# Kernel tuning notes

Measured on AMD Instinct MI355X. Metric: run time of the kernel, lower is better.

## Reference

```python
import jax, jax.numpy as jnp
import numpy as np

N = 100000       # nodes
E = 1600000      # edges (avg degree 16)
F_IN = 128
F_HID = 64
F_OUT = 40
K = 10
ALPHA = 0.1


def setup_inputs() -> dict:
    key = jax.random.key(0)
    k1, k2, k3, k4, k5, k6 = jax.random.split(key, 6)
    x = jax.random.normal(k1, (N, F_IN), dtype=jnp.float32)
    edge_index = jax.random.randint(k2, (2, E), 0, N, dtype=jnp.int32)
    # Linear params (Kaiming-uniform-ish scale)
    W1 = jax.random.normal(k3, (F_IN, F_HID), dtype=jnp.float32) / np.sqrt(F_IN)
    b1 = jax.random.normal(k4, (F_HID,), dtype=jnp.float32) * 0.01
    W2 = jax.random.normal(k5, (F_HID, F_OUT), dtype=jnp.float32) / np.sqrt(F_HID)
    b2 = jax.random.normal(k6, (F_OUT,), dtype=jnp.float32) * 0.01
    return {"x": x, "edge_index": edge_index, "W1": W1, "b1": b1, "W2": W2, "b2": b2}


def _gcn_norm(edge_index, dtype):
    # add self loops, symmetric normalization D^{-1/2} (A+I) D^{-1/2}
    loops = jnp.arange(N, dtype=edge_index.dtype)
    src = jnp.concatenate([edge_index[0], loops])
    dst = jnp.concatenate([edge_index[1], loops])
    deg = jax.ops.segment_sum(jnp.ones_like(src, dtype=dtype), dst, num_segments=N)
    dinv = jnp.where(deg > 0, jax.lax.rsqrt(deg), 0.0).astype(dtype)
    norm = dinv[src] * dinv[dst]  # [E + N]
    return src, dst, norm


def _appnp(x, src, dst, norm):
    h = x  # teleport target
    def step(xc, _):
        agg = jax.ops.segment_sum(xc[src] * norm[:, None], dst, num_segments=N)
        return (1.0 - ALPHA) * agg + ALPHA * h, None
    out, _ = jax.lax.scan(step, x, None, length=K)
    return out


def reference(x, edge_index, W1, b1, W2, b2):
    src, dst, norm = _gcn_norm(edge_index, x.dtype)
    # layer 1: Linear -> relu -> (dropout p=0) -> APPNP
    h = jax.nn.relu(x @ W1 + b1)
    h = _appnp(h, src, dst, norm)
    # layer 2: Linear -> relu -> APPNP
    h = jax.nn.relu(h @ W2 + b2)
    h = _appnp(h, src, dst, norm)
    return jax.nn.log_softmax(h, axis=1)
```

## Files before the change

kernel.cpp:

```cpp
#include <hip/hip_runtime.h>
#include <hip/hip_fp16.h>
#include <hip/hip_fp8.h>

namespace {
constexpr int NN = 100000;
constexpr int NE = 1600000;
constexpr int FIN = 128, FHID = 64, FOUT = 40;
constexpr float ALPHA = 0.1f;
constexpr int SLOTS = 64;
constexpr int SB = 40;
constexpr int ECHUNK = 200000;

typedef int v4i __attribute__((ext_vector_type(4)));
typedef unsigned int v2u __attribute__((ext_vector_type(2)));
typedef unsigned int v4u __attribute__((ext_vector_type(4)));
typedef float v2f __attribute__((ext_vector_type(2)));
typedef float v4f __attribute__((ext_vector_type(4)));
typedef _Float16 half8 __attribute__((ext_vector_type(8)));

#if __has_builtin(__builtin_amdgcn_cvt_pk_f32_fp8) && __has_builtin(__builtin_amdgcn_cvt_pk_fp8_f32)
#define HW_FP8 1
#else
#define HW_FP8 0
#endif

__device__ __forceinline__ ushort f2h(float v) {
  union { __half h; ushort u; } cv;
  cv.h = __float2half_rn(v);
  return cv.u;
}

__device__ __forceinline__ void acc8_fp8(v2u w, float* a) {
#if HW_FP8
  v2f p0 = __builtin_amdgcn_cvt_pk_f32_fp8((int)w.x, false);
  v2f p1 = __builtin_amdgcn_cvt_pk_f32_fp8((int)w.x, true);
  v2f p2 = __builtin_amdgcn_cvt_pk_f32_fp8((int)w.y, false);
  v2f p3 = __builtin_amdgcn_cvt_pk_f32_fp8((int)w.y, true);
  a[0] += p0.x; a[1] += p0.y; a[2] += p1.x; a[3] += p1.y;
  a[4] += p2.x; a[5] += p2.y; a[6] += p3.x; a[7] += p3.y;
#else
  union { v2u w; unsigned char b[8]; } cv;
  cv.w = w;
#pragma unroll
  for (int k = 0; k < 8; k++) {
    __hip_fp8_e4m3 h;
    h.__x = cv.b[k];
    a[k] += (float)h;
  }
#endif
}

__device__ __forceinline__ v2u enc8_fp8(const float* o) {
#if HW_FP8
  int d0 = __builtin_amdgcn_cvt_pk_fp8_f32(o[0], o[1], 0, false);
  d0 = __builtin_amdgcn_cvt_pk_fp8_f32(o[2], o[3], d0, true);
  int d1 = __builtin_amdgcn_cvt_pk_fp8_f32(o[4], o[5], 0, false);
  d1 = __builtin_amdgcn_cvt_pk_fp8_f32(o[6], o[7], d1, true);
  v2u r;
  r.x = (unsigned int)d0;
  r.y = (unsigned int)d1;
  return r;
#else
  union { v2u w; unsigned char b[8]; } cv;
#pragma unroll
  for (int k = 0; k < 8; k++) {
    __hip_fp8_e4m3 h(o[k]);
    cv.b[k] = h.__x;
  }
  return cv.w;
#endif
}

__device__ __forceinline__ unsigned int enc4_fp8(float a, float b, float c, float d) {
#if HW_FP8
  int d0 = __builtin_amdgcn_cvt_pk_fp8_f32(a, b, 0, false);
  d0 = __builtin_amdgcn_cvt_pk_fp8_f32(c, d, d0, true);
  return (unsigned int)d0;
#else
  union { unsigned char b4[4]; unsigned int u; } cv;
  __hip_fp8_e4m3 h0(a), h1(b), h2(c), h3(d);
  cv.b4[0] = h0.__x; cv.b4[1] = h1.__x; cv.b4[2] = h2.__x; cv.b4[3] = h3.__x;
  return cv.u;
#endif
}

__global__ void k_zero(int* cnt) {
  int i = blockIdx.x * 256 + threadIdx.x;
  if (i < NN) cnt[i] = 0;
}

__global__ void k_fill_ell(const int* __restrict__ src, const int* __restrict__ dst,
                           int* __restrict__ cnt, int* __restrict__ ell, int ebase) {
  int e = ebase + blockIdx.x * 256 + threadIdx.x;
  if (e >= ebase + ECHUNK || e >= NE) return;
  int s = src[e], d = dst[e];
  int p = atomicAdd(&cnt[d], 1);
  if (p < SLOTS) ell[(size_t)p * NN + d] = s;
}

__global__ void k_dinv(const int* __restrict__ cnt, float2* __restrict__ dd) {
  int i = blockIdx.x * 256 + threadIdx.x;
  if (i < NN) {
    float di = rsqrtf((float)(cnt[i] + 1));
    dd[i] = make_float2(di, 0.9f * di * di);
  }
}

__global__ __launch_bounds__(256, 3) void k_mlp(const float* __restrict__ x,
                                                const float* __restrict__ W1,
                                                const float* __restrict__ b1,
                                                const float* __restrict__ W2,
                                                const float2* __restrict__ dd,
                                                float* __restrict__ h2x,
                                                ushort* __restrict__ u0,
                                                unsigned char* __restrict__ uq) {
  __shared__ _Float16 w1t[64 * 136];
  __shared__ _Float16 w2t[48 * 72];
  __shared__ unsigned int ht[4 * 16 * 36];

  int tid = threadIdx.x;
  for (int i = tid; i < 2048; i += 256) {
    float4 v = ((const float4*)W1)[i];
    int k = i >> 4;
    int c0 = (i & 15) * 4;
    w1t[(c0 + 0) * 136 + k] = (_Float16)v.x;
    w1t[(c0 + 1) * 136 + k] = (_Float16)v.y;
    w1t[(c0 + 2) * 136 + k] = (_Float16)v.z;
    w1t[(c0 + 3) * 136 + k] = (_Float16)v.w;
  }
  for (int i = tid; i < 2560; i += 256) {
    int k = i / 40, c = i - k * 40;
    w2t[c * 72 + k] = (_Float16)W2[i];
  }
  for (int i = tid; i < 576; i += 256) w2t[2880 + i] = (_Float16)0.f;
  __syncthreads();

  int wid = tid >> 6, lane = tid & 63;
  int g = lane >> 4, n = lane & 15;
  int node = blockIdx.x * 64 + wid * 16 + n;
  int nodeL = node < NN ? node : NN - 1;
  const float* xr = x + (size_t)nodeL * FIN;

  v4f acc1[4] = {};
#pragma unroll
  for (int kk = 0; kk < 4; kk++) {
    const float4* xp = (const float4*)(xr + kk * 32 + g * 8);
    float4 xa = xp[0], xb = xp[1];
    half8 bx;
    bx[0] = (_Float16)xa.x; bx[1] = (_Float16)xa.y;
    bx[2] = (_Float16)xa.z; bx[3] = (_Float16)xa.w;
    bx[4] = (_Float16)xb.x; bx[5] = (_Float16)xb.y;
    bx[6] = (_Float16)xb.z; bx[7] = (_Float16)xb.w;
#pragma unroll
    for (int mt = 0; mt < 4; mt++) {
      half8 af = *(const half8*)(w1t + (mt * 16 + n) * 136 + kk * 32 + g * 8);
      acc1[mt] = __builtin_amdgcn_mfma_f32_16x16x32_f16(af, bx, acc1[mt], 0, 0, 0);
    }
  }

  unsigned int* hw = ht + wid * 576 + n * 36;
#pragma unroll
  for (int mt = 0; mt < 4; mt++) {
    float4 bb = *(const float4*)(b1 + mt * 16 + g * 4);
    union { _Float16 h[4]; uint2 u; } pk;
    pk.h[0] = (_Float16)fmaxf(acc1[mt][0] + bb.x, 0.f);
    pk.h[1] = (_Float16)fmaxf(acc1[mt][1] + bb.y, 0.f);
    pk.h[2] = (_Float16)fmaxf(acc1[mt][2] + bb.z, 0.f);
    pk.h[3] = (_Float16)fmaxf(acc1[mt][3] + bb.w, 0.f);
    *(uint2*)(hw + mt * 8 + g * 2) = pk.u;
  }

  v4f acc2[3] = {};
#pragma unroll
  for (int kk = 0; kk < 2; kk++) {
    half8 bh = *(const half8*)((const _Float16*)(hw + kk * 16 + g * 4));
#pragma unroll
    for (int mt2 = 0; mt2 < 3; mt2++) {
      half8 af = *(const half8*)(w2t + (mt2 * 16 + n) * 72 + kk * 32 + g * 8);
      acc2[mt2] = __builtin_amdgcn_mfma_f32_16x16x32_f16(af, bh, acc2[mt2], 0, 0, 0);
    }
  }

  if (node < NN) {
    float di = dd[node].x;
#pragma unroll
    for (int mt2 = 0; mt2 < 3; mt2++) {
      int c0 = mt2 * 16 + g * 4;
      if (c0 < FOUT) {
        float y0 = acc2[mt2][0], y1 = acc2[mt2][1];
        float y2 = acc2[mt2][2], y3 = acc2[mt2][3];
        *(float4*)(h2x + (size_t)node * FOUT + c0) = make_float4(y0, y1, y2, y3);
        float u0v = di * y0, u1v = di * y1, u2v = di * y2, u3v = di * y3;
        union { ushort s[4]; uint2 q; } hq;
        hq.s[0] = f2h(u0v); hq.s[1] = f2h(u1v);
        hq.s[2] = f2h(u2v); hq.s[3] = f2h(u3v);
        *(uint2*)(u0 + (size_t)node * FOUT + c0) = hq.q;
        *(unsigned int*)(uq + (size_t)node * SB + c0) = enc4_fp8(u0v, u1v, u2v, u3v);
      }
    }
  }
}

__device__ __forceinline__ void gather_pm(const int* __restrict__ ell,
                                          const unsigned char* __restrict__ u,
                                          int node, int ch, int deg, float* a) {
#pragma unroll
  for (int k = 0; k < 8; k++) a[k] = 0.f;
  const unsigned char* ub = u + ch * 8;
  v2u ws = *(const v2u*)(ub + (size_t)node * SB);
  int q[8], qn[8];
#pragma unroll
  for (int k = 0; k < 8; k++) q[k] = ell[(size_t)k * NN + node];
  acc8_fp8(ws, a);
  int j = 0;
  for (; j + 8 <= deg; j += 8) {
#pragma unroll
    for (int k = 0; k < 8; k++) {
      int pl = j + 8 + k;
      pl = pl > SLOTS - 1 ? SLOTS - 1 : pl;
      qn[k] = ell[(size_t)pl * NN + node];
    }
    v2u w[8];
#pragma unroll
    for (int k = 0; k < 8; k++) w[k] = *(const v2u*)(ub + (size_t)q[k] * SB);
#pragma unroll
    for (int k = 0; k < 8; k++) acc8_fp8(w[k], a);
#pragma unroll
    for (int k = 0; k < 8; k++) q[k] = qn[k];
  }
  int rr = deg - j;
#pragma unroll
  for (int k = 0; k < 7; k++) {
    if (k < rr) acc8_fp8(*(const v2u*)(ub + (size_t)q[k] * SB), a);
  }
}

#define APPNP_HDR(cntp)                            \
  int tid = threadIdx.x;                           \
  int nd = tid / 5, ch = tid - nd * 5;             \
  int node = blockIdx.x * 64 + nd;                 \
  if (node >= NN) return;                          \
  int deg = (cntp)[node];                          \
  deg = deg > SLOTS ? SLOTS : deg;

__device__ __forceinline__ void store_h8(ushort* p, const float* v) {
  union { v4u u; __half h[8]; } cv;
#pragma unroll
  for (int k = 0; k < 8; k++) cv.h[k] = __float2half_rn(v[k]);
  *(v4u*)p = cv.u;
}

__global__ __launch_bounds__(320, 6) void k_mid(const int* __restrict__ cnt,
                                                const int* __restrict__ ell,
                                                const float2* __restrict__ dd,
                                                const ushort* __restrict__ u0,
                                                const unsigned char* __restrict__ u,
                                                unsigned char* __restrict__ un) {
  APPNP_HDR(cnt)
  union { v4u q; __half h[8]; } t0;
  t0.q = *(const v4u*)(u0 + (size_t)node * FOUT + ch * 8);
  float c9 = dd[node].y;
  float a[8];
  gather_pm(ell, u, node, ch, deg, a);
  float o[8];
#pragma unroll
  for (int k = 0; k < 8; k++) o[k] = c9 * a[k] + ALPHA * __half2float(t0.h[k]);
  v2u st = enc8_fp8(o);
  *(v2u*)(un + (size_t)node * SB + ch * 8) = st;
}

__global__ __launch_bounds__(320, 6) void k_final1(const int* __restrict__ cnt,
                                                   const int* __restrict__ ell,
                                                   const float2* __restrict__ dd,
                                                   const float* __restrict__ b2,
                                                   const float* __restrict__ h2x,
                                                   const unsigned char* __restrict__ u,
                                                   ushort* __restrict__ gh,
                                                   ushort* __restrict__ u0n,
                                                   unsigned char* __restrict__ uqn) {
  APPNP_HDR(cnt)
  float di = dd[node].x;
  v4f h0 = __builtin_nontemporal_load((const v4f*)(h2x + (size_t)node * FOUT + ch * 8));
  v4f h1 = __builtin_nontemporal_load((const v4f*)(h2x + (size_t)node * FOUT + ch * 8 + 4));
  const float* bb = b2 + ch * 8;
  float a[8];
  gather_pm(ell, u, node, ch, deg, a);
  float t9 = 0.9f * di;
  float hx[8] = {h0.x, h0.y, h0.z, h0.w, h1.x, h1.y, h1.z, h1.w};
  float g[8], ug[8];
#pragma unroll
  for (int k = 0; k < 8; k++) {
    float z = t9 * a[k] + ALPHA * hx[k] + bb[k];
    g[k] = fmaxf(z, 0.f);
    ug[k] = di * g[k];
  }
  store_h8(gh + (size_t)node * FOUT + ch * 8, g);
  store_h8(u0n + (size_t)node * FOUT + ch * 8, ug);
  v2u st = enc8_fp8(ug);
  *(v2u*)(uqn + (size_t)node * SB + ch * 8) = st;
}

__global__ __launch_bounds__(320, 6) void k_final2(const int* __restrict__ cnt,
                                                   const int* __restrict__ ell,
                                                   const float2* __restrict__ dd,
                                                   const ushort* __restrict__ gh,
                                                   const unsigned char* __restrict__ u,
                                                   ushort* __restrict__ zh) {
  APPNP_HDR(cnt)
  union { v4u q; __half h[8]; } hv;
  hv.q = *(const v4u*)(gh + (size_t)node * FOUT + ch * 8);
  float t9 = 0.9f * dd[node].x;
  float a[8];
  gather_pm(ell, u, node, ch, deg, a);
  float o[8];
#pragma unroll
  for (int k = 0; k < 8; k++) o[k] = t9 * a[k] + ALPHA * __half2float(hv.h[k]);
  store_h8(zh + (size_t)node * FOUT + ch * 8, o);
}

__global__ void k_logsoftmax(const ushort* __restrict__ in, float* __restrict__ out) {
  int i = blockIdx.x * 256 + threadIdx.x;
  if (i >= NN) return;
  union { v4u q; __half h[8]; } v[5];
  const v4u* r = (const v4u*)(in + (size_t)i * FOUT);
  float f[40];
  float m = -1e30f;
#pragma unroll
  for (int j = 0; j < 5; j++) {
    v[j].q = r[j];
#pragma unroll
    for (int k = 0; k < 8; k++) {
      f[j * 8 + k] = __half2float(v[j].h[k]);
      m = fmaxf(m, f[j * 8 + k]);
    }
  }
  float sum = 0.f;
#pragma unroll
  for (int j = 0; j < 40; j++) sum += expf(f[j] - m);
  float lse = m + logf(sum);
  float4* o = (float4*)(out + (size_t)i * FOUT);
#pragma unroll
  for (int j = 0; j < 10; j++) {
    float4 w = {f[j * 4] - lse, f[j * 4 + 1] - lse, f[j * 4 + 2] - lse, f[j * 4 + 3] - lse};
    o[j] = w;
  }
}

}

extern "C" void kernel_launch(void* const* d_in, const int* in_sizes, int n_in,
                              void* d_out, int out_size, void* d_ws, size_t ws_size,
                              hipStream_t stream) {
  const float* x = (const float*)d_in[0];
  const int* ei = (const int*)d_in[1];
  const int* src = ei;
  const int* dst = ei + NE;
  const float* W1 = (const float*)d_in[2];
  const float* b1 = (const float*)d_in[3];
  const float* W2 = (const float*)d_in[4];
  const float* b2 = (const float*)d_in[5];
  float* out = (float*)d_out;

  char* ws = (char*)d_ws;
  size_t off = 0;
  auto alloc = [&](size_t bytes) -> void* {
    void* p = ws + off;
    off += (bytes + 255) & ~(size_t)255;
    return p;
  };
  int* cnt          = (int*)alloc((size_t)NN * 4);
  float2* dd        = (float2*)alloc((size_t)NN * 8);
  int* ell          = (int*)alloc((size_t)NN * SLOTS * 4);
  float* h2x        = (float*)alloc((size_t)NN * FOUT * 4);
  ushort* u0h       = (ushort*)alloc((size_t)NN * FOUT * 2);
  ushort* gh        = (ushort*)alloc((size_t)NN * FOUT * 2);
  ushort* zh        = (ushort*)alloc((size_t)NN * FOUT * 2);
  unsigned char* q0 = (unsigned char*)alloc((size_t)NN * SB);
  unsigned char* qA = (unsigned char*)alloc((size_t)NN * SB);
  unsigned char* qB = (unsigned char*)alloc((size_t)NN * SB);

  k_zero<<<(NN + 255) / 256, 256, 0, stream>>>(cnt);
  for (int c = 0; c < NE / ECHUNK; c++)
    k_fill_ell<<<(ECHUNK + 255) / 256, 256, 0, stream>>>(src, dst, cnt, ell, c * ECHUNK);
  k_dinv<<<(NN + 255) / 256, 256, 0, stream>>>(cnt, dd);

  k_mlp<<<(NN + 63) / 64, 256, 0, stream>>>(x, W1, b1, W2, dd, h2x, u0h, q0);

  int agrid = (NN + 63) / 64;
  const unsigned char* cu = q0;
  for (int it = 0; it < 9; it++) {
    unsigned char* nx = (it & 1) ? qB : qA;
    k_mid<<<agrid, 320, 0, stream>>>(cnt, ell, dd, u0h, cu, nx);
    cu = nx;
  }
  k_final1<<<agrid, 320, 0, stream>>>(cnt, ell, dd, b2, h2x, cu, gh, u0h, q0);

  cu = q0;
  for (int it = 0; it < 9; it++) {
    unsigned char* nx = (it & 1) ? qB : qA;
    k_mid<<<agrid, 320, 0, stream>>>(cnt, ell, dd, u0h, cu, nx);
    cu = nx;
  }
  k_final2<<<agrid, 320, 0, stream>>>(cnt, ell, dd, gh, cu, zh);

  k_logsoftmax<<<(NN + 255) / 256, 256, 0, stream>>>(zh, out);
}
```

Before: 638.3 us.

## Fuse all APPNP propagation steps into one persistent cooperative kernel

New measurement: 639.9 us. About the same (+0.2%).

```diff
diff --git a/kernel.cpp b/kernel.cpp
--- a/kernel.cpp
+++ b/kernel.cpp
@@ -1,6 +1,9 @@
 #include <hip/hip_runtime.h>
 #include <hip/hip_fp16.h>
 #include <hip/hip_fp8.h>
+#include <hip/hip_cooperative_groups.h>
+
+namespace cg = cooperative_groups;
 
 namespace {
 constexpr int NN = 100000;
@@ -10,6 +13,8 @@
 constexpr int SLOTS = 64;
 constexpr int SB = 40;
 constexpr int ECHUNK = 200000;
+constexpr int GPB = 102;
+constexpr int NCH = (NN + GPB - 1) / GPB;
 
 typedef int v4i __attribute__((ext_vector_type(4)));
 typedef unsigned int v2u __attribute__((ext_vector_type(2)));
@@ -198,6 +203,134 @@
         *(unsigned int*)(uq + (size_t)node * SB + c0) = enc4_fp8(u0v, u1v, u2v, u3v);
       }
     }
+  }
+}
+
+__global__ __launch_bounds__(512, 8) void k_appnp_all(
+    const int* __restrict__ cnt, const int* __restrict__ ell,
+    const float2* __restrict__ dd, ushort* __restrict__ u0,
+    const float* __restrict__ b2, const float* __restrict__ h2x,
+    ushort* __restrict__ zh,
+    unsigned char* __restrict__ q0, unsigned char* __restrict__ qA,
+    unsigned char* __restrict__ qB) {
+  __shared__ int sidx[GPB][SLOTS + 1];
+  __shared__ int sdeg[GPB];
+
+  int tid = threadIdx.x;
+  int base = blockIdx.x * GPB;
+  if (tid < GPB) {
+    int n = base + tid;
+    int d = (n < NN) ? cnt[n] : 0;
+    sdeg[tid] = d > SLOTS ? SLOTS : d;
+  }
+  __syncthreads();
+  for (int i = tid; i < GPB * SLOTS; i += 512) {
+    int p = i / GPB, n = i - p * GPB;
+    int node = base + n;
+    if (node < NN && p < sdeg[n]) sidx[n][p] = ell[(size_t)p * NN + node];
+  }
+  __syncthreads();
+
+  int nd = tid / 5, ch = tid - nd * 5;
+  int node = base + nd;
+  bool act = (nd < GPB) && (node < NN);
+  int deg = act ? sdeg[nd] : 0;
+  float di = 0.f, c9 = 0.f;
+  if (act) {
+    float2 d2 = dd[node];
+    di = d2.x;
+    c9 = d2.y;
+  }
+  union { v4u q; __half h[8]; } t0;
+  if (act) t0.q = *(const v4u*)(u0 + (size_t)node * FOUT + ch * 8);
+
+  cg::grid_group grid = cg::this_grid();
+
+  auto gather = [&](const unsigned char* u, float* a) {
+    const unsigned char* ub = u + ch * 8;
+#pragma unroll
+    for (int k = 0; k < 8; k++) a[k] = 0.f;
+    acc8_fp8(*(const v2u*)(ub + (size_t)node * SB), a);
+    int j = 0;
+    for (; j + 8 <= deg; j += 8) {
+      v2u w[8];
+#pragma unroll
+      for (int k = 0; k < 8; k++)
+        w[k] = *(const v2u*)(ub + (size_t)sidx[nd][j + k] * SB);
+#pragma unroll
+      for (int k = 0; k < 8; k++) acc8_fp8(w[k], a);
+    }
+    for (; j < deg; j++)
+      acc8_fp8(*(const v2u*)(ub + (size_t)sidx[nd][j] * SB), a);
+  };
+
+  const unsigned char* cu = q0;
+  for (int it = 0; it < 9; it++) {
+    unsigned char* nx = (it & 1) ? qB : qA;
+    if (act) {
+      float a[8];
+      gather(cu, a);
+      float o[8];
+#pragma unroll
+      for (int k = 0; k < 8; k++) o[k] = c9 * a[k] + ALPHA * __half2float(t0.h[k]);
+      *(v2u*)(nx + (size_t)node * SB + ch * 8) = enc8_fp8(o);
+    }
+    __threadfence();
+    grid.sync();
+    cu = nx;
+  }
+
+  union { v4u q; __half h[8]; } ghr;
+  if (act) {
+    float a[8];
+    gather(cu, a);
+    v4f h0 = *(const v4f*)(h2x + (size_t)node * FOUT + ch * 8);
+    v4f h1 = *(const v4f*)(h2x + (size_t)node * FOUT + ch * 8 + 4);
+    const float* bb = b2 + ch * 8;
+    float hx[8] = {h0.x, h0.y, h0.z, h0.w, h1.x, h1.y, h1.z, h1.w};
+    float t9 = 0.9f * di;
+    float g[8], ug[8];
+#pragma unroll
+    for (int k = 0; k < 8; k++) {
+      float z = t9 * a[k] + ALPHA * hx[k] + bb[k];
+      g[k] = fmaxf(z, 0.f);
+      ug[k] = di * g[k];
+    }
+#pragma unroll
+    for (int k = 0; k < 8; k++) {
+      ghr.h[k] = __float2half_rn(g[k]);
+      t0.h[k] = __float2half_rn(ug[k]);
+    }
+    *(v2u*)(q0 + (size_t)node * SB + ch * 8) = enc8_fp8(ug);
+  }
+  __threadfence();
+  grid.sync();
+
+  cu = q0;
+  for (int it = 0; it < 9; it++) {
+    unsigned char* nx = (it & 1) ? qB : qA;
+    if (act) {
+      float a[8];
+      gather(cu, a);
+      float o[8];
+#pragma unroll
+      for (int k = 0; k < 8; k++) o[k] = c9 * a[k] + ALPHA * __half2float(t0.h[k]);
+      *(v2u*)(nx + (size_t)node * SB + ch * 8) = enc8_fp8(o);
+    }
+    __threadfence();
+    grid.sync();
+    cu = nx;
+  }
+
+  if (act) {
+    float a[8];
+    gather(cu, a);
+    float t9 = 0.9f * di;
+    union { v4u u4; __half h[8]; } cv;
+#pragma unroll
+    for (int k = 0; k < 8; k++)
+      cv.h[k] = __float2half_rn(t9 * a[k] + ALPHA * __half2float(ghr.h[k]));
+    *(v4u*)(zh + (size_t)node * FOUT + ch * 8) = cv.u4;
   }
 }
 
@@ -386,22 +519,34 @@
 
   k_mlp<<<(NN + 63) / 64, 256, 0, stream>>>(x, W1, b1, W2, dd, h2x, u0h, q0);
 
-  int agrid = (NN + 63) / 64;
-  const unsigned char* cu = q0;
-  for (int it = 0; it < 9; it++) {
-    unsigned char* nx = (it & 1) ? qB : qA;
-    k_mid<<<agrid, 320, 0, stream>>>(cnt, ell, dd, u0h, cu, nx);
-    cu = nx;
-  }
-  k_final1<<<agrid, 320, 0, stream>>>(cnt, ell, dd, b2, h2x, cu, gh, u0h, q0);
-
-  cu = q0;
-  for (int it = 0; it < 9; it++) {
-    unsigned char* nx = (it & 1) ? qB : qA;
-    k_mid<<<agrid, 320, 0, stream>>>(cnt, ell, dd, u0h, cu, nx);
-    cu = nx;
-  }
-  k_final2<<<agrid, 320, 0, stream>>>(cnt, ell, dd, gh, cu, zh);
+  static int coopTotal = -1;
+  if (coopTotal < 0) {
+    int nb = 0;
+    hipOccupancyMaxActiveBlocksPerMultiprocessor(&nb, k_appnp_all, 512, 0);
+    coopTotal = nb * 256;
+  }
+  if (coopTotal >= NCH) {
+    void* kargs[] = {(void*)&cnt, (void*)&ell, (void*)&dd,  (void*)&u0h,
+                     (void*)&b2,  (void*)&h2x, (void*)&zh,  (void*)&q0,
+                     (void*)&qA,  (void*)&qB};
+    hipLaunchCooperativeKernel((void*)k_appnp_all, dim3(NCH), dim3(512), kargs, 0, stream);
+  } else {
+    int agrid = (NN + 63) / 64;
+    const unsigned char* cu = q0;
+    for (int it = 0; it < 9; it++) {
+      unsigned char* nx = (it & 1) ? qB : qA;
+      k_mid<<<agrid, 320, 0, stream>>>(cnt, ell, dd, u0h, cu, nx);
+      cu = nx;
+    }
+    k_final1<<<agrid, 320, 0, stream>>>(cnt, ell, dd, b2, h2x, cu, gh, u0h, q0);
+    cu = q0;
+    for (int it = 0; it < 9; it++) {
+      unsigned char* nx = (it & 1) ? qB : qA;
+      k_mid<<<agrid, 320, 0, stream>>>(cnt, ell, dd, u0h, cu, nx);
+      cu = nx;
+    }
+    k_final2<<<agrid, 320, 0, stream>>>(cnt, ell, dd, gh, cu, zh);
+  }
 
   k_logsoftmax<<<(NN + 255) / 256, 256, 0, stream>>>(zh, out);
 }
```

## Merge ELL fill and MLP into one launch, split degree scaling into separate kernel

Applied to the files above, without the earlier changes.

Measured after the change: 671.8 us. 5.2% more time.

```diff
diff --git a/kernel.cpp b/kernel.cpp
--- a/kernel.cpp
+++ b/kernel.cpp
@@ -9,7 +9,8 @@
 constexpr float ALPHA = 0.1f;
 constexpr int SLOTS = 64;
 constexpr int SB = 40;
-constexpr int ECHUNK = 200000;
+constexpr int NFILL = NE / 256;
+constexpr int NMLP = (NN + 63) / 64;
 
 typedef int v4i __attribute__((ext_vector_type(4)));
 typedef unsigned int v2u __attribute__((ext_vector_type(2)));
@@ -71,31 +72,9 @@
 #endif
 }
 
-__device__ __forceinline__ unsigned int enc4_fp8(float a, float b, float c, float d) {
-#if HW_FP8
-  int d0 = __builtin_amdgcn_cvt_pk_fp8_f32(a, b, 0, false);
-  d0 = __builtin_amdgcn_cvt_pk_fp8_f32(c, d, d0, true);
-  return (unsigned int)d0;
-#else
-  union { unsigned char b4[4]; unsigned int u; } cv;
-  __hip_fp8_e4m3 h0(a), h1(b), h2(c), h3(d);
-  cv.b4[0] = h0.__x; cv.b4[1] = h1.__x; cv.b4[2] = h2.__x; cv.b4[3] = h3.__x;
-  return cv.u;
-#endif
-}
-
 __global__ void k_zero(int* cnt) {
   int i = blockIdx.x * 256 + threadIdx.x;
   if (i < NN) cnt[i] = 0;
-}
-
-__global__ void k_fill_ell(const int* __restrict__ src, const int* __restrict__ dst,
-                           int* __restrict__ cnt, int* __restrict__ ell, int ebase) {
-  int e = ebase + blockIdx.x * 256 + threadIdx.x;
-  if (e >= ebase + ECHUNK || e >= NE) return;
-  int s = src[e], d = dst[e];
-  int p = atomicAdd(&cnt[d], 1);
-  if (p < SLOTS) ell[(size_t)p * NN + d] = s;
 }
 
 __global__ void k_dinv(const int* __restrict__ cnt, float2* __restrict__ dd) {
@@ -106,19 +85,30 @@
   }
 }
 
-__global__ __launch_bounds__(256, 3) void k_mlp(const float* __restrict__ x,
-                                                const float* __restrict__ W1,
-                                                const float* __restrict__ b1,
-                                                const float* __restrict__ W2,
-                                                const float2* __restrict__ dd,
-                                                float* __restrict__ h2x,
-                                                ushort* __restrict__ u0,
-                                                unsigned char* __restrict__ uq) {
+__global__ __launch_bounds__(256, 3) void k_build(const int* __restrict__ src,
+                                                  const int* __restrict__ dst,
+                                                  int* __restrict__ cnt,
+                                                  int* __restrict__ ell,
+                                                  const float* __restrict__ x,
+                                                  const float* __restrict__ W1,
+                                                  const float* __restrict__ b1,
+                                                  const float* __restrict__ W2,
+                                                  float* __restrict__ h2x) {
   __shared__ _Float16 w1t[64 * 136];
   __shared__ _Float16 w2t[48 * 72];
   __shared__ unsigned int ht[4 * 16 * 36];
 
   int tid = threadIdx.x;
+
+  if (blockIdx.x < NFILL) {
+    int e = blockIdx.x * 256 + tid;
+    int s = src[e], d = dst[e];
+    int p = atomicAdd(&cnt[d], 1);
+    if (p < SLOTS) ell[(size_t)p * NN + d] = s;
+    return;
+  }
+
+  int mb = blockIdx.x - NFILL;
   for (int i = tid; i < 2048; i += 256) {
     float4 v = ((const float4*)W1)[i];
     int k = i >> 4;
@@ -137,7 +127,7 @@
 
   int wid = tid >> 6, lane = tid & 63;
   int g = lane >> 4, n = lane & 15;
-  int node = blockIdx.x * 64 + wid * 16 + n;
+  int node = mb * 64 + wid * 16 + n;
   int nodeL = node < NN ? node : NN - 1;
   const float* xr = x + (size_t)nodeL * FIN;
 
@@ -182,23 +172,35 @@
   }
 
   if (node < NN) {
-    float di = dd[node].x;
 #pragma unroll
     for (int mt2 = 0; mt2 < 3; mt2++) {
       int c0 = mt2 * 16 + g * 4;
       if (c0 < FOUT) {
-        float y0 = acc2[mt2][0], y1 = acc2[mt2][1];
-        float y2 = acc2[mt2][2], y3 = acc2[mt2][3];
-        *(float4*)(h2x + (size_t)node * FOUT + c0) = make_float4(y0, y1, y2, y3);
-        float u0v = di * y0, u1v = di * y1, u2v = di * y2, u3v = di * y3;
-        union { ushort s[4]; uint2 q; } hq;
-        hq.s[0] = f2h(u0v); hq.s[1] = f2h(u1v);
-        hq.s[2] = f2h(u2v); hq.s[3] = f2h(u3v);
-        *(uint2*)(u0 + (size_t)node * FOUT + c0) = hq.q;
-        *(unsigned int*)(uq + (size_t)node * SB + c0) = enc4_fp8(u0v, u1v, u2v, u3v);
+        *(float4*)(h2x + (size_t)node * FOUT + c0) =
+            make_float4(acc2[mt2][0], acc2[mt2][1], acc2[mt2][2], acc2[mt2][3]);
       }
     }
   }
+}
+
+__global__ __launch_bounds__(320) void k_scale(const float2* __restrict__ dd,
+                                               const float* __restrict__ h2x,
+                                               ushort* __restrict__ u0,
+                                               unsigned char* __restrict__ uq) {
+  int tid = threadIdx.x;
+  int nd = tid / 5, ch = tid - nd * 5;
+  int node = blockIdx.x * 64 + nd;
+  if (node >= NN) return;
+  float di = dd[node].x;
+  v4f h0 = *(const v4f*)(h2x + (size_t)node * FOUT + ch * 8);
+  v4f h1 = *(const v4f*)(h2x + (size_t)node * FOUT + ch * 8 + 4);
+  float u[8] = {di * h0.x, di * h0.y, di * h0.z, di * h0.w,
+                di * h1.x, di * h1.y, di * h1.z, di * h1.w};
+  union { v4u q; __half h[8]; } cv;
+#pragma unroll
+  for (int k = 0; k < 8; k++) cv.h[k] = __float2half_rn(u[k]);
+  *(v4u*)(u0 + (size_t)node * FOUT + ch * 8) = cv.q;
+  *(v2u*)(uq + (size_t)node * SB + ch * 8) = enc8_fp8(u);
 }
 
 __device__ __forceinline__ void gather_pm(const int* __restrict__ ell,
@@ -380,11 +382,9 @@
   unsigned char* qB = (unsigned char*)alloc((size_t)NN * SB);
 
   k_zero<<<(NN + 255) / 256, 256, 0, stream>>>(cnt);
-  for (int c = 0; c < NE / ECHUNK; c++)
-    k_fill_ell<<<(ECHUNK + 255) / 256, 256, 0, stream>>>(src, dst, cnt, ell, c * ECHUNK);
+  k_build<<<NFILL + NMLP, 256, 0, stream>>>(src, dst, cnt, ell, x, W1, b1, W2, h2x);
   k_dinv<<<(NN + 255) / 256, 256, 0, stream>>>(cnt, dd);
-
-  k_mlp<<<(NN + 63) / 64, 256, 0, stream>>>(x, W1, b1, W2, dd, h2x, u0h, q0);
+  k_scale<<<(NN + 63) / 64, 320, 0, stream>>>(dd, h2x, u0h, q0);
 
   int agrid = (NN + 63) / 64;
   const unsigned char* cu = q0;
```
